# Kernel tuning notes

Hardware: AMD Instinct MI355X
Metric: run time of the kernel (lower is better)

The kernel has to match this reference:

```python
import jax, jax.numpy as jnp
import numpy as np
from jax import lax

B, C, H, W = 4, 64, 256, 256
CH = C // 2  # attention hidden channels


def conv2d_same(x, w, b):
    # x: [B,Ci,H,W], w: [Co,Ci,kh,kw]
    y = lax.conv_general_dilated(x, w, (1, 1), 'SAME',
                                 dimension_numbers=('NCHW', 'OIHW', 'NCHW'))
    return y + b[None, :, None, None]


def conv1x1(x, w):
    # w: [Co,Ci]
    return jnp.einsum('oi,bihw->bohw', w, x)


def irnn_scan(x, w, b, axis, reverse):
    """Directional IRNN: h_t = relu(x_t + w_c * h_{t-1} + b_c), per channel.
    axis: 2 (rows/H) or 3 (cols/W). reverse=True scans from the far edge
    (e.g. bottom-to-top for 'up', right-to-left for 'left')."""
    xs = jnp.moveaxis(x, axis, 0)            # [L, B, C, rest]
    wb = w[None, :, None]                    # broadcast over [B, C, rest]
    bb = b[None, :, None]

    def step(h, xt):
        h = jax.nn.relu(xt + wb * h + bb)
        return h, h

    h0 = jnp.zeros_like(xs[0])
    _, ys = lax.scan(step, h0, xs, reverse=reverse)
    return jnp.moveaxis(ys, 0, axis)


def setup_inputs() -> dict:
    key = jax.random.key(0)
    ks = jax.random.split(key, 16)
    d = {}
    d['x'] = jax.random.normal(ks[0], (B, C, H, W), dtype=jnp.float32)
    # conv_in: 1x1, no bias
    d['w_in'] = jax.random.normal(ks[1], (C, C), dtype=jnp.float32) * 0.05
    # IRNN depthwise 1x1 weights (init alpha=1.0 in torch) + biases
    for i, name in enumerate(['up', 'right', 'down', 'left']):
        d['w_' + name] = jnp.ones((C,), dtype=jnp.float32)
        d['b_' + name] = jax.random.normal(ks[2 + i], (C,), dtype=jnp.float32) * 0.01
    # convD2: 1x1, 4C -> C, no bias
    d['wD2'] = jax.random.normal(ks[6], (C, 4 * C), dtype=jnp.float32) * 0.01
    # attention layers
    d['a1_w'] = jax.random.normal(ks[7], (CH, C, 3, 3), dtype=jnp.float32) * 0.05
    d['a1_b'] = jnp.zeros((CH,), dtype=jnp.float32)
    d['a2_w'] = jax.random.normal(ks[8], (CH, CH, 3, 3), dtype=jnp.float32) * 0.05
    d['a2_b'] = jnp.zeros((CH,), dtype=jnp.float32)
    d['a3_w'] = jax.random.normal(ks[9], (1, CH), dtype=jnp.float32) * 0.05
    d['a3_b'] = jnp.zeros((1,), dtype=jnp.float32)
    return d


def reference(x, w_in, w_up, b_up, w_right, b_right, w_down, b_down,
              w_left, b_left, wD2, a1_w, a1_b, a2_w, a2_b, a3_w, a3_b):
    out = conv1x1(x, w_in)
    # four directional spatial IRNN scans
    top_up = irnn_scan(out, w_up, b_up, axis=2, reverse=True)     # bottom->top
    top_right = irnn_scan(out, w_right, b_right, axis=3, reverse=False)  # left->right
    top_down = irnn_scan(out, w_down, b_down, axis=2, reverse=False)     # top->bottom
    top_left = irnn_scan(out, w_left, b_left, axis=3, reverse=True)      # right->left
    cat = jnp.concatenate([top_up, top_right, top_down, top_left], axis=1)  # [B,4C,H,W]
    out = jax.nn.relu(conv1x1(cat, wD2))
    # attention gate
    a = jax.nn.relu(conv2d_same(out, a1_w, a1_b))
    a = jax.nn.relu(conv2d_same(a, a2_w, a2_b))
    a = conv1x1(a, a3_w) + a3_b[None, :, None, None]
    weight = jax.nn.sigmoid(a)                # [B,1,H,W]
    return jax.nn.relu(x * weight)
```

## Files before the change

kernel.cpp:

```cpp
#include <hip/hip_runtime.h>
#include <hip/hip_bf16.h>

#define HWSZ  65536

typedef unsigned short ushort_t;
typedef unsigned int   uint_t;
typedef __attribute__((ext_vector_type(8))) _Float16 half8;
typedef __attribute__((ext_vector_type(4))) float f32x4;

static __device__ __forceinline__ void gl_lds16(const void* g, void* l) {
    __builtin_amdgcn_global_load_lds(
        (const __attribute__((address_space(1))) unsigned int*)g,
        (__attribute__((address_space(3))) unsigned int*)l, 16, 0, 0);
}

__global__ __launch_bounds__(256) void k1_conv1x1(
    const float* __restrict__ x, const float* __restrict__ w_in,
    float* __restrict__ out0)
{
    __shared__ float xs[64][64];
    int b   = blockIdx.x >> 10;
    int hw0 = (blockIdx.x & 1023) << 6;
    const float* xb = x + ((size_t)b * 64) * HWSZ + hw0;

    for (int idx = threadIdx.x; idx < 1024; idx += 256) {
        int i = idx >> 4, p4 = (idx & 15) << 2;
        *(float4*)&xs[i][p4] = *(const float4*)(xb + (size_t)i * HWSZ + p4);
    }
    __syncthreads();

    int p  = threadIdx.x & 63;
    int og = __builtin_amdgcn_readfirstlane(threadIdx.x >> 6);
    float acc[16];
#pragma unroll
    for (int oo = 0; oo < 16; oo++) acc[oo] = 0.f;

#pragma unroll 8
    for (int i = 0; i < 64; i++) {
        float xv = xs[i][p];
#pragma unroll
        for (int oo = 0; oo < 16; oo++)
            acc[oo] += w_in[(og * 16 + oo) * 64 + i] * xv;
    }
    float* ob = out0 + ((size_t)b * HWSZ + hw0 + p) * 64 + og * 16;
#pragma unroll
    for (int k = 0; k < 4; k++) {
        float4 v = {acc[4*k], acc[4*k+1], acc[4*k+2], acc[4*k+3]};
        *(float4*)(ob + 4*k) = v;
    }
}

__global__ __launch_bounds__(256) void k2_scan(
    const float* __restrict__ out0,
    const float* __restrict__ w_up, const float* __restrict__ b_up,
    const float* __restrict__ w_rt, const float* __restrict__ b_rt,
    const float* __restrict__ w_dn, const float* __restrict__ b_dn,
    const float* __restrict__ w_lf, const float* __restrict__ b_lf,
    _Float16* __restrict__ cat)
{
    int c = threadIdx.x & 63;
    int q = threadIdx.x >> 6;
    int dir = blockIdx.x >> 8;
    int bid = blockIdx.x & 255;
    int b = bid >> 6, g = bid & 63;
    int line = g * 4 + q;
    size_t base = (size_t)b * HWSZ;

    float wv, bv; int coff;
    if      (dir == 0) { wv = w_dn[c]; bv = b_dn[c]; coff = 128; }
    else if (dir == 1) { wv = w_up[c]; bv = b_up[c]; coff = 0;   }
    else if (dir == 2) { wv = w_rt[c]; bv = b_rt[c]; coff = 64;  }
    else               { wv = w_lf[c]; bv = b_lf[c]; coff = 192; }
    bool fwd  = (dir == 0) || (dir == 2);
    bool vert = (dir <= 1);

    float h = 0.f;
    for (int k0 = 0; k0 < 256; k0 += 8) {
        float v[8];
#pragma unroll
        for (int j = 0; j < 8; j++) {
            int i = fwd ? (k0 + j) : 255 - (k0 + j);
            size_t pix = vert ? (base + i * 256 + line) : (base + line * 256 + i);
            v[j] = out0[pix * 64 + c];
        }
#pragma unroll
        for (int j = 0; j < 8; j++) {
            int i = fwd ? (k0 + j) : 255 - (k0 + j);
            size_t pix = vert ? (base + i * 256 + line) : (base + line * 256 + i);
            h = fmaxf(0.f, v[j] + wv * h + bv);
            cat[pix * 256 + coff + c] = (_Float16)h;
        }
    }
}

__global__ __launch_bounds__(256) void packw(const float* __restrict__ wD2,
                                             _Float16* __restrict__ wf)
{
    int i = blockIdx.x * 256 + threadIdx.x;
    wf[i] = (_Float16)wD2[i];
}

__global__ __launch_bounds__(256) void packb(
    const float* __restrict__ a1w, const float* __restrict__ a2w,
    _Float16* __restrict__ p1, _Float16* __restrict__ p2)
{
    int i = blockIdx.x * 256 + threadIdx.x;
    if (i < 18432) {
        int j = i & 7, lane = (i >> 3) & 63, st = i >> 9;
        int s = st >> 1, t = st & 1;
        int oc = t * 16 + (lane & 15);
        int gk = s * 32 + (lane >> 4) * 8 + j;
        int dydx = gk >> 6, ic = gk & 63;
        p1[i] = (_Float16)a1w[((oc * 64 + ic) * 3 + dydx / 3) * 3 + dydx % 3];
    } else if (i < 27648) {
        int e = i - 18432;
        int j = e & 7, lane = (e >> 3) & 63, st = e >> 9;
        int s = st >> 1, t = st & 1;
        int oc = t * 16 + (lane & 15);
        int gk = s * 32 + (lane >> 4) * 8 + j;
        int dydx = gk >> 5, ic = gk & 31;
        p2[e] = (_Float16)a2w[((oc * 32 + ic) * 3 + dydx / 3) * 3 + dydx % 3];
    }
}

__global__ __launch_bounds__(256) void k3_mfma(
    const _Float16* __restrict__ cat, const _Float16* __restrict__ wf,
    _Float16* __restrict__ out3)
{
    __shared__ _Float16 As[64 * 256];
    int wave = threadIdx.x >> 6, lane = threadIdx.x & 63;
    int n16 = lane & 15, quad = lane >> 4;
    size_t p0 = (size_t)blockIdx.x * 64;

    half8 B[8];
#pragma unroll
    for (int s = 0; s < 8; s++)
        B[s] = *(const half8*)(wf + (size_t)(wave * 16 + n16) * 256 + s * 32 + quad * 8);

#pragma unroll
    for (int it = 0; it < 8; it++) {
        int px = wave * 16 + it * 2 + (lane >> 5);
        int pu = lane & 31;
        int lu = pu ^ (px & 7);
        const _Float16* gp = cat + ((p0 + px) << 8) + lu * 8;
        _Float16* lp = As + wave * 4096 + it * 512;
        gl_lds16(gp, lp);
    }
    __syncthreads();

    f32x4 acc[4] = {};
#pragma unroll
    for (int j = 0; j < 4; j++) {
        int px = j * 16 + n16;
        const _Float16* lrow = As + px * 256;
        int x7 = px & 7;
#pragma unroll
        for (int s = 0; s < 8; s++) {
            int phys = (s * 4 + quad) ^ x7;
            half8 a = *(const half8*)(lrow + phys * 8);
            acc[j] = __builtin_amdgcn_mfma_f32_16x16x32_f16(a, B[s], acc[j], 0, 0, 0);
        }
    }

#pragma unroll
    for (int j = 0; j < 4; j++)
#pragma unroll
        for (int r = 0; r < 4; r++) {
            size_t op = (p0 + j * 16 + quad * 4 + r) * 64 + wave * 16 + n16;
            out3[op] = (_Float16)fmaxf(acc[j][r], 0.f);
        }
}

template <int IC>
__global__ __launch_bounds__(256) void convmfma(
    const _Float16* __restrict__ in, const _Float16* __restrict__ pb,
    const float* __restrict__ bias, _Float16* __restrict__ oh)
{
    constexpr int UPX = IC / 8;
    constexpr int KST = IC / 32;
    constexpr int PPS = 64 / UPX;
    __shared__ _Float16 Ls[6 * 66 * IC];

    int wave = threadIdx.x >> 6, lane = threadIdx.x & 63;
    int n16 = lane & 15, quad = lane >> 4;
    int bid = blockIdx.x;
    int bb  = bid >> 8;
    int hh0 = ((bid >> 2) & 63) << 2;
    int w0  = (bid & 3) << 6;
    const _Float16* ib = in + (size_t)bb * HWSZ * IC;

#pragma unroll
    for (int it = 0; it < (6 * UPX) / 4; it++) {
        int q   = it * 4 + wave;
        int r   = q / UPX, seg = q % UPX;
        int gh  = hh0 - 1 + r;
        int pxr = seg * PPS + lane / UPX;
        int pu  = lane % UPX;
        int px_lin = r * 66 + 1 + pxr;
        int lu  = (UPX == 8) ? (pu ^ (px_lin & 7)) : pu;
        _Float16* lp = Ls + (size_t)(r * 66 + 1 + seg * PPS) * IC;
        if ((unsigned)gh < 256u) {
            const _Float16* gp = ib + ((size_t)(gh * 256 + w0 + pxr)) * IC + lu * 8;
            gl_lds16(gp, lp);
        } else {
            half8 z = {};
            *(half8*)(lp + (size_t)lane * 8) = z;
        }
    }
    if (threadIdx.x < 12 * UPX) {
        int pu = threadIdx.x % UPX;
        int ph = threadIdx.x / UPX;
        int r = ph >> 1, side = ph & 1;
        int col = side ? 65 : 0;
        int gh = hh0 - 1 + r;
        int gw = w0 - 1 + side * 65;
        int px_lin = r * 66 + col;
        int lu = (UPX == 8) ? (pu ^ (px_lin & 7)) : pu;
        half8 v = {};
        if ((unsigned)gh < 256u && (unsigned)gw < 256u)
            v = *(const half8*)(ib + ((size_t)(gh * 256 + gw)) * IC + lu * 8);
        *(half8*)(Ls + (size_t)px_lin * IC + pu * 8) = v;
    }
    __syncthreads();

    f32x4 acc[4][2] = {};
#pragma unroll
    for (int dydx = 0; dydx < 9; dydx++) {
        int dy = dydx / 3, dx = dydx % 3;
        int r_lds = wave + dy;
#pragma unroll
        for (int kst = 0; kst < KST; kst++) {
            int s = dydx * KST + kst;
            half8 B0 = *(const half8*)(pb + (size_t)((s * 2 + 0) * 64 + lane) * 8);
            half8 B1 = *(const half8*)(pb + (size_t)((s * 2 + 1) * 64 + lane) * 8);
            int u = kst * 4 + quad;
#pragma unroll
            for (int j = 0; j < 4; j++) {
                int px_lin = r_lds * 66 + j * 16 + n16 + dx;
                int phys = (UPX == 8) ? (u ^ (px_lin & 7)) : u;
                half8 A = *(const half8*)(Ls + (size_t)px_lin * IC + phys * 8);
                acc[j][0] = __builtin_amdgcn_mfma_f32_16x16x32_f16(A, B0, acc[j][0], 0, 0, 0);
                acc[j][1] = __builtin_amdgcn_mfma_f32_16x16x32_f16(A, B1, acc[j][1], 0, 0, 0);
            }
        }
    }

    int hh = hh0 + wave;
#pragma unroll
    for (int t = 0; t < 2; t++) {
        float bv = bias[t * 16 + n16];
#pragma unroll
        for (int j = 0; j < 4; j++)
#pragma unroll
            for (int r = 0; r < 4; r++) {
                int wp = w0 + j * 16 + quad * 4 + r;
                size_t op = ((size_t)bb * HWSZ + hh * 256 + wp) * 32 + t * 16 + n16;
                oh[op] = (_Float16)fmaxf(acc[j][t][r] + bv, 0.f);
            }
    }
}

__global__ __launch_bounds__(256) void k6_gate(
    const _Float16* __restrict__ a2, const float* __restrict__ a3w,
    const float* __restrict__ a3b, const float* __restrict__ x,
    float* __restrict__ out)
{
    int pix = blockIdx.x * 256 + threadIdx.x;
    int b = pix >> 16;
    int hw = pix & 65535;
    const _Float16* ap = a2 + (size_t)pix * 32;
    half8 q0 = *(const half8*)(ap);
    half8 q1 = *(const half8*)(ap + 8);
    half8 q2 = *(const half8*)(ap + 16);
    half8 q3 = *(const half8*)(ap + 24);
    float s = a3b[0];
#pragma unroll
    for (int j = 0; j < 8; j++) {
        s += a3w[j]      * (float)q0[j];
        s += a3w[j + 8]  * (float)q1[j];
        s += a3w[j + 16] * (float)q2[j];
        s += a3w[j + 24] * (float)q3[j];
    }
    float g = 1.f / (1.f + __expf(-s));
    const float* xb = x + (size_t)b * 64 * HWSZ + hw;
    float* ob = out + (size_t)b * 64 * HWSZ + hw;
#pragma unroll 8
    for (int c = 0; c < 64; c++)
        ob[(size_t)c * HWSZ] = fmaxf(0.f, xb[(size_t)c * HWSZ] * g);
}

extern "C" void kernel_launch(void* const* d_in, const int* in_sizes, int n_in,
                              void* d_out, int out_size, void* d_ws, size_t ws_size,
                              hipStream_t stream)
{
    const float* x     = (const float*)d_in[0];
    const float* w_in  = (const float*)d_in[1];
    const float* w_up  = (const float*)d_in[2];
    const float* b_up  = (const float*)d_in[3];
    const float* w_rt  = (const float*)d_in[4];
    const float* b_rt  = (const float*)d_in[5];
    const float* w_dn  = (const float*)d_in[6];
    const float* b_dn  = (const float*)d_in[7];
    const float* w_lf  = (const float*)d_in[8];
    const float* b_lf  = (const float*)d_in[9];
    const float* wD2   = (const float*)d_in[10];
    const float* a1w   = (const float*)d_in[11];
    const float* a1b   = (const float*)d_in[12];
    const float* a2w   = (const float*)d_in[13];
    const float* a2b   = (const float*)d_in[14];
    const float* a3w   = (const float*)d_in[15];
    const float* a3b   = (const float*)d_in[16];
    float* out = (float*)d_out;

    char* ws = (char*)d_ws;
    float*    out0 = (float*)ws;
    _Float16* out3 = (_Float16*)ws;
    _Float16* wf16 = (_Float16*)(ws + (33ull << 20));
    _Float16* p1   = (_Float16*)(ws + (34ull << 20));
    _Float16* p2   = (_Float16*)(ws + (35ull << 20));
    _Float16* cat  = (_Float16*)(ws + (64ull << 20));
    _Float16* a1   = (_Float16*)(ws + (64ull << 20));
    _Float16* a2   = (_Float16*)(ws + (80ull << 20));

    k1_conv1x1<<<4096, 256, 0, stream>>>(x, w_in, out0);
    k2_scan   <<<1024, 256, 0, stream>>>(out0, w_up, b_up, w_rt, b_rt,
                                         w_dn, b_dn, w_lf, b_lf, cat);
    packw     <<<64,   256, 0, stream>>>(wD2, wf16);
    packb     <<<108,  256, 0, stream>>>(a1w, a2w, p1, p2);
    k3_mfma   <<<4096, 256, 0, stream>>>(cat, wf16, out3);
    convmfma<64><<<1024, 256, 0, stream>>>(out3, p1, a1b, a1);
    convmfma<32><<<1024, 256, 0, stream>>>(a1, p2, a2b, a2);
    k6_gate   <<<1024, 256, 0, stream>>>(a2, a3w, a3b, x, out);
}
```

Measured before the change: 322.7 us.

## Use split-fp16 MFMA for input 1x1 conv, store fp16, fuse scan direction pairs

The input 1x1 convolution now runs on MFMA, using a hi/lo fp16 split of activations and weights (three MFMAs per step) to keep near-fp32 accuracy. Its output is stored as fp16 instead of fp32, halving the intermediate write and the scan's read traffic. The scan kernel now runs the two opposite directions on each axis inside one block, so each line's data is read twice by the same block and likely hits in cache. The costs are less parallelism in the scan (512 blocks instead of 1024) and fp16 rounding of the intermediate.

```diff
diff --git a/kernel.cpp b/kernel.cpp
--- a/kernel.cpp
+++ b/kernel.cpp
@@ -14,44 +14,66 @@
         (__attribute__((address_space(3))) unsigned int*)l, 16, 0, 0);
 }
 
-__global__ __launch_bounds__(256) void k1_conv1x1(
+__global__ __launch_bounds__(256) void k1_mfma(
     const float* __restrict__ x, const float* __restrict__ w_in,
-    float* __restrict__ out0)
+    _Float16* __restrict__ out0)
 {
     __shared__ float xs[64][64];
     int b   = blockIdx.x >> 10;
     int hw0 = (blockIdx.x & 1023) << 6;
     const float* xb = x + ((size_t)b * 64) * HWSZ + hw0;
+    int wave = threadIdx.x >> 6, lane = threadIdx.x & 63;
+    int n16 = lane & 15, quad = lane >> 4;
 
     for (int idx = threadIdx.x; idx < 1024; idx += 256) {
         int i = idx >> 4, p4 = (idx & 15) << 2;
         *(float4*)&xs[i][p4] = *(const float4*)(xb + (size_t)i * HWSZ + p4);
     }
+
+    half8 Bh[2], Bl[2];
+#pragma unroll
+    for (int s = 0; s < 2; s++) {
+        const float* wp = w_in + (wave * 16 + n16) * 64 + s * 32 + quad * 8;
+#pragma unroll
+        for (int j = 0; j < 8; j++) {
+            float v = wp[j];
+            _Float16 h = (_Float16)v;
+            float r = v - (float)h;
+            Bh[s][j] = h; Bl[s][j] = (_Float16)r;
+        }
+    }
     __syncthreads();
 
-    int p  = threadIdx.x & 63;
-    int og = __builtin_amdgcn_readfirstlane(threadIdx.x >> 6);
-    float acc[16];
-#pragma unroll
-    for (int oo = 0; oo < 16; oo++) acc[oo] = 0.f;
-
-#pragma unroll 8
-    for (int i = 0; i < 64; i++) {
-        float xv = xs[i][p];
-#pragma unroll
-        for (int oo = 0; oo < 16; oo++)
-            acc[oo] += w_in[(og * 16 + oo) * 64 + i] * xv;
-    }
-    float* ob = out0 + ((size_t)b * HWSZ + hw0 + p) * 64 + og * 16;
-#pragma unroll
-    for (int k = 0; k < 4; k++) {
-        float4 v = {acc[4*k], acc[4*k+1], acc[4*k+2], acc[4*k+3]};
-        *(float4*)(ob + 4*k) = v;
-    }
+    f32x4 acc[4] = {};
+#pragma unroll
+    for (int j = 0; j < 4; j++) {
+#pragma unroll
+        for (int s = 0; s < 2; s++) {
+            half8 Ah, Al;
+#pragma unroll
+            for (int jj = 0; jj < 8; jj++) {
+                float v = xs[s * 32 + quad * 8 + jj][j * 16 + n16];
+                _Float16 h = (_Float16)v;
+                float r = v - (float)h;
+                Ah[jj] = h; Al[jj] = (_Float16)r;
+            }
+            acc[j] = __builtin_amdgcn_mfma_f32_16x16x32_f16(Ah, Bh[s], acc[j], 0, 0, 0);
+            acc[j] = __builtin_amdgcn_mfma_f32_16x16x32_f16(Al, Bh[s], acc[j], 0, 0, 0);
+            acc[j] = __builtin_amdgcn_mfma_f32_16x16x32_f16(Ah, Bl[s], acc[j], 0, 0, 0);
+        }
+    }
+    _Float16* ob = out0 + ((size_t)b * HWSZ + hw0) * 64 + wave * 16;
+#pragma unroll
+    for (int j = 0; j < 4; j++)
+#pragma unroll
+        for (int r = 0; r < 4; r++) {
+            int px = j * 16 + quad * 4 + r;
+            ob[(size_t)px * 64 + n16] = (_Float16)acc[j][r];
+        }
 }
 
 __global__ __launch_bounds__(256) void k2_scan(
-    const float* __restrict__ out0,
+    const _Float16* __restrict__ out0,
     const float* __restrict__ w_up, const float* __restrict__ b_up,
     const float* __restrict__ w_rt, const float* __restrict__ b_rt,
     const float* __restrict__ w_dn, const float* __restrict__ b_dn,
@@ -60,35 +82,38 @@
 {
     int c = threadIdx.x & 63;
     int q = threadIdx.x >> 6;
-    int dir = blockIdx.x >> 8;
+    bool vert = blockIdx.x < 256;
     int bid = blockIdx.x & 255;
     int b = bid >> 6, g = bid & 63;
     int line = g * 4 + q;
     size_t base = (size_t)b * HWSZ;
 
-    float wv, bv; int coff;
-    if      (dir == 0) { wv = w_dn[c]; bv = b_dn[c]; coff = 128; }
-    else if (dir == 1) { wv = w_up[c]; bv = b_up[c]; coff = 0;   }
-    else if (dir == 2) { wv = w_rt[c]; bv = b_rt[c]; coff = 64;  }
-    else               { wv = w_lf[c]; bv = b_lf[c]; coff = 192; }
-    bool fwd  = (dir == 0) || (dir == 2);
-    bool vert = (dir <= 1);
-
-    float h = 0.f;
-    for (int k0 = 0; k0 < 256; k0 += 8) {
-        float v[8];
-#pragma unroll
-        for (int j = 0; j < 8; j++) {
-            int i = fwd ? (k0 + j) : 255 - (k0 + j);
-            size_t pix = vert ? (base + i * 256 + line) : (base + line * 256 + i);
-            v[j] = out0[pix * 64 + c];
-        }
-#pragma unroll
-        for (int j = 0; j < 8; j++) {
-            int i = fwd ? (k0 + j) : 255 - (k0 + j);
-            size_t pix = vert ? (base + i * 256 + line) : (base + line * 256 + i);
-            h = fmaxf(0.f, v[j] + wv * h + bv);
-            cat[pix * 256 + coff + c] = (_Float16)h;
+    float w0v, b0v, w1v, b1v; int coff0, coff1;
+    if (vert) { w0v = w_dn[c]; b0v = b_dn[c]; coff0 = 128;
+                w1v = w_up[c]; b1v = b_up[c]; coff1 = 0; }
+    else      { w0v = w_rt[c]; b0v = b_rt[c]; coff0 = 64;
+                w1v = w_lf[c]; b1v = b_lf[c]; coff1 = 192; }
+
+#pragma unroll
+    for (int pass = 0; pass < 2; pass++) {
+        float wv = pass ? w1v : w0v, bv = pass ? b1v : b0v;
+        int coff = pass ? coff1 : coff0;
+        float h = 0.f;
+        for (int k0 = 0; k0 < 256; k0 += 8) {
+            float v[8];
+#pragma unroll
+            for (int jx = 0; jx < 8; jx++) {
+                int i = pass ? 255 - (k0 + jx) : (k0 + jx);
+                size_t pix = vert ? (base + i * 256 + line) : (base + line * 256 + i);
+                v[jx] = (float)out0[pix * 64 + c];
+            }
+#pragma unroll
+            for (int jx = 0; jx < 8; jx++) {
+                int i = pass ? 255 - (k0 + jx) : (k0 + jx);
+                size_t pix = vert ? (base + i * 256 + line) : (base + line * 256 + i);
+                h = fmaxf(0.f, v[jx] + wv * h + bv);
+                cat[pix * 256 + coff + c] = (_Float16)h;
+            }
         }
     }
 }
@@ -313,7 +338,7 @@
     float* out = (float*)d_out;
 
     char* ws = (char*)d_ws;
-    float*    out0 = (float*)ws;
+    _Float16* out0 = (_Float16*)ws;
     _Float16* out3 = (_Float16*)ws;
     _Float16* wf16 = (_Float16*)(ws + (33ull << 20));
     _Float16* p1   = (_Float16*)(ws + (34ull << 20));
@@ -322,8 +347,8 @@
     _Float16* a1   = (_Float16*)(ws + (64ull << 20));
     _Float16* a2   = (_Float16*)(ws + (80ull << 20));
 
-    k1_conv1x1<<<4096, 256, 0, stream>>>(x, w_in, out0);
-    k2_scan   <<<1024, 256, 0, stream>>>(out0, w_up, b_up, w_rt, b_rt,
+    k1_mfma   <<<4096, 256, 0, stream>>>(x, w_in, out0);
+    k2_scan   <<<512,  256, 0, stream>>>(out0, w_up, b_up, w_rt, b_rt,
                                          w_dn, b_dn, w_lf, b_lf, cat);
     packw     <<<64,   256, 0, stream>>>(wD2, wf16);
     packb     <<<108,  256, 0, stream>>>(a1w, a2w, p1, p2);
```

After: 277.8 us. -13.9%, faster.
